# Performance work log

Hardware: AMD Instinct MI355X
Metric: run time of the kernel (lower is better)

## Reference

```python
import jax, jax.numpy as jnp
import numpy as np

NUM_CLASSES = 19
VIEWS = 50          # views_per_class: min(min_views, max_views_per_class)=50, no max_features_total cap (38*50<=10000)
TEMP = 0.1
CM_TEMP = 0.1
EPS = 1e-12


def setup_inputs() -> dict:
    key = jax.random.key(0)
    k1, k2, k3 = jax.random.split(key, 3)
    label = jax.random.randint(k1, (2, 512, 1024), 0, NUM_CLASSES)
    color_fea = jax.random.normal(k2, (2, 256, 128, 256), dtype=jnp.float32)
    other_fea = jax.random.normal(k3, (2, 256, 128, 256), dtype=jnp.float32)
    return {"label": label, "color_fea": color_fea, "other_fea": other_fea}


def _sample(compare, feature):
    # compare: [N, Cc, HW] bool (pixel belongs to class), feature: [N, C, HW]
    # random per-class sampling of VIEWS pixels: argsort random keys restricted to class pixels
    n, cc, hw = compare.shape
    rand = jax.random.uniform(jax.random.key(42), (n, hw))
    keys = jnp.where(compare, rand[:, None, :], 2.0)          # non-class pixels pushed to the end
    idx = jnp.argsort(keys, axis=-1)[:, :, :VIEWS]            # [N, Cc, V]
    samp = jnp.take_along_axis(feature[:, None, :, :], idx[:, :, None, :], axis=-1)  # [N, Cc, C, V]
    c = feature.shape[1]
    return samp.reshape(n * cc, c, VIEWS)                     # [T, C, V]


def _norm_flat(feats):
    # feats: [T, C, V] -> l2-normalize over C, transpose, flatten to [T*V, C]
    f = feats / jnp.maximum(jnp.linalg.norm(feats, axis=1, keepdims=True), EPS)
    t, c, v = f.shape
    return jnp.transpose(f, (0, 2, 1)).reshape(t * v, c)


def _masks(labels_flat):
    m = (labels_flat[:, None] == labels_flat[None, :]).astype(jnp.float32)
    neg = 1.0 - m
    pos = m * (1.0 - jnp.eye(m.shape[0], dtype=m.dtype))      # exclude self from positives
    return pos, neg


def _infonce(dot, pos, neg):
    exp = jnp.exp(dot)
    neg_logits = (exp * neg).sum(1, keepdims=True)
    log_prob = dot - jnp.log(exp + neg_logits)
    pos_sums = pos.sum(1)
    norm = jnp.where(pos_sums > 0, pos_sums, 1.0)
    return -(((pos * log_prob).sum(1)) / norm).mean()


def reference(label, color_fea, other_fea):
    n, h, w = label.shape
    scale = w // color_fea.shape[-1]
    # nearest-neighbour downsample of label to feature resolution (torch interpolate 'nearest' with integer factor)
    ld = label[:, ::scale, ::scale].reshape(n, -1)                       # [N, HW]
    compare = ld[:, None, :] == jnp.arange(NUM_CLASSES)[None, :, None]   # [N, Cc, HW]
    cf = color_fea.reshape(n, color_fea.shape[1], -1)
    of = other_fea.reshape(n, other_fea.shape[1], -1)
    fc = _sample(compare, cf)                                            # [T, C, V]
    fo = _sample(compare, of)
    labels = jnp.tile(jnp.arange(NUM_CLASSES), n).astype(jnp.float32)    # [T]
    labels_flat = jnp.repeat(labels, VIEWS)                              # [T*V]
    pos, neg = _masks(labels_flat)
    fcf = _norm_flat(fc)
    fof = _norm_flat(fo)
    loss_cm = _infonce(fcf @ fof.T / CM_TEMP, pos, neg)
    loss_vis = _infonce(fcf @ fcf.T / TEMP, pos, neg)
    loss_aux = _infonce(fof @ fof.T / TEMP, pos, neg)
    return (loss_cm, loss_vis, loss_aux)
```

## Files before the change

### kernel.cpp

```cpp
#include <hip/hip_runtime.h>
#include <hip/hip_bf16.h>
#include <cstdint>
#include <cstddef>

#define HW    32768
#define NCLS  19
#define VIEWS 50
#define NT    38
#define NR    1900
#define NRP   1920
#define CH    256
#define CAP   3072

#define OFF_LD   65536u
#define OFF_SEL  131072u
#define OFF_CNT  133120u
#define OFF_KEYS 133184u
#define OFF_FCF  366656u
#define OFF_FOF  612416u
#define OFF_NEG  858176u
#define OFF_POS  863936u

typedef __attribute__((ext_vector_type(8))) short short8;
typedef __attribute__((ext_vector_type(4))) float f32x4;

__device__ __forceinline__ unsigned rotl32(unsigned x, int d) {
    return (x << d) | (x >> (32 - d));
}

__global__ __launch_bounds__(256) void prep_kernel(const int* __restrict__ label,
                                                   int* __restrict__ ld,
                                                   int* __restrict__ counts,
                                                   unsigned long long* __restrict__ keys,
                                                   float* __restrict__ negsum,
                                                   float* __restrict__ out) {
    int tid = threadIdx.x;
    int j = blockIdx.x * 256 + tid;
    unsigned x0 = (unsigned)j, x1 = (unsigned)(j + HW);
    const unsigned ks0 = 0u, ks1 = 42u, ks2 = 0x1BD11BDAu ^ 0u ^ 42u;
    x0 += ks0; x1 += ks1;
#define TF_RND(r) { x0 += x1; x1 = rotl32(x1, r); x1 ^= x0; }
    TF_RND(13) TF_RND(15) TF_RND(26) TF_RND(6)   x0 += ks1; x1 += ks2 + 1u;
    TF_RND(17) TF_RND(29) TF_RND(16) TF_RND(24)  x0 += ks2; x1 += ks0 + 2u;
    TF_RND(13) TF_RND(15) TF_RND(26) TF_RND(6)   x0 += ks0; x1 += ks1 + 3u;
    TF_RND(17) TF_RND(29) TF_RND(16) TF_RND(24)  x0 += ks1; x1 += ks2 + 4u;
    TF_RND(13) TF_RND(15) TF_RND(26) TF_RND(6)   x0 += ks2; x1 += ks0 + 5u;
#undef TF_RND
    float r0 = __uint_as_float((x0 >> 9) | 0x3f800000u) - 1.0f;
    float r1 = __uint_as_float((x1 >> 9) | 0x3f800000u) - 1.0f;
    int y = j >> 8, x = j & 255;
    int off = (y << 2) * 1024 + (x << 2);
    int c0 = label[off];
    int c1 = label[512 * 1024 + off];
    ld[j]      = c0;
    ld[HW + j] = c1;
    if (j < 3 * NR) negsum[j] = 0.0f;
    if (j < 3) out[j] = 0.0f;

    __shared__ int lcnt[NT], lbase[NT];
    if (tid < NT) lcnt[tid] = 0;
    __syncthreads();
    int t0 = c0, t1 = NCLS + c1;
    int p0 = atomicAdd(&lcnt[t0], 1);
    int p1 = atomicAdd(&lcnt[t1], 1);
    __syncthreads();
    if (tid < NT) {
        int c = lcnt[tid];
        lbase[tid] = (c > 0) ? atomicAdd(&counts[tid], c) : 0;
    }
    __syncthreads();
    int s0 = lbase[t0] + p0;
    int s1 = lbase[t1] + p1;
    if (s0 < CAP)
        keys[(size_t)t0 * CAP + s0] = (((unsigned long long)__float_as_uint(r0)) << 32) | (unsigned)j;
    if (s1 < CAP)
        keys[(size_t)t1 * CAP + s1] = (((unsigned long long)__float_as_uint(r1)) << 32) | (unsigned)j;
}

__global__ __launch_bounds__(256) void select_kernel(const int* __restrict__ counts,
                                                     const unsigned long long* __restrict__ keys,
                                                     const int* __restrict__ ld,
                                                     int* __restrict__ sel) {
    int t = blockIdx.x;
    int tid = threadIdx.x;
    int cnt = min(counts[t], CAP);
    const unsigned long long* g = keys + (size_t)t * CAP;
    __shared__ unsigned hist[256];
    __shared__ unsigned long long cand[256];
    __shared__ int s_B, s_nbelow, s_ncand;
    hist[tid] = 0;
    if (tid == 0) { s_B = 256; s_nbelow = 0; s_ncand = 0; }
    __syncthreads();

    unsigned long long kreg[12];
    int binreg[12];
    int nk = 0;
    for (int p = tid; p < cnt; p += 256) {
        unsigned long long k = g[p];
        unsigned v = (unsigned)(__uint_as_float((unsigned)(k >> 32)) * 8388608.0f);
        int b = (int)(v >> 15);
        kreg[nk] = k; binreg[nk] = b; nk++;
        atomicAdd(&hist[b], 1u);
    }
    __syncthreads();

    if (cnt >= VIEWS) {
        for (int s = 1; s < 256; s <<= 1) {
            unsigned add = (tid >= s) ? hist[tid - s] : 0u;
            unsigned cur = hist[tid];
            __syncthreads();
            hist[tid] = cur + add;
            __syncthreads();
        }
        unsigned cum  = hist[tid];
        unsigned prev = (tid > 0) ? hist[tid - 1] : 0u;
        if (cum >= VIEWS && prev < VIEWS) s_B = tid;
        __syncthreads();
        int B = s_B;
        for (int q = 0; q < nk; ++q) {
            if (binreg[q] < B) {
                int pos = atomicAdd(&s_nbelow, 1);
                if (pos < VIEWS) sel[t * VIEWS + pos] = (int)(kreg[q] & 0xffffffffu);
            } else if (binreg[q] == B) {
                int pos = atomicAdd(&s_ncand, 1);
                if (pos < 256) cand[pos] = kreg[q];
            }
        }
        __syncthreads();
        int nbelow = s_nbelow;
        int need   = VIEWS - nbelow;
        int ncand  = min(s_ncand, 256);
        if (tid < 64) {
            unsigned long long r0 = (tid       < ncand) ? cand[tid]       : ~0ull;
            unsigned long long r1 = (tid + 64  < ncand) ? cand[tid + 64]  : ~0ull;
            unsigned long long r2 = (tid + 128 < ncand) ? cand[tid + 128] : ~0ull;
            unsigned long long r3 = (tid + 192 < ncand) ? cand[tid + 192] : ~0ull;
            for (int v = 0; v < need; ++v) {
                unsigned long long a = (r0 < r1) ? r0 : r1;
                unsigned long long b = (r2 < r3) ? r2 : r3;
                unsigned long long best = (a < b) ? a : b;
                for (int m = 32; m >= 1; m >>= 1) {
                    unsigned long long o = __shfl_xor(best, m);
                    if (o < best) best = o;
                }
                if (tid == 0) sel[t * VIEWS + nbelow + v] = (int)(best & 0xffffffffu);
                if (r0 == best) r0 = ~0ull;
                if (r1 == best) r1 = ~0ull;
                if (r2 == best) r2 = ~0ull;
                if (r3 == best) r3 = ~0ull;
            }
        }
    } else {
        for (int q = 0; q < nk; ++q) {
            int pos = atomicAdd(&s_nbelow, 1);
            if (pos < VIEWS) sel[t * VIEWS + pos] = (int)(kreg[q] & 0xffffffffu);
        }
        __syncthreads();
        if (tid == 0) {
            int fill = s_nbelow;
            int n = t / NCLS, c = t % NCLS;
            const int* ldn = ld + n * HW;
            for (int j = 0; j < HW && fill < VIEWS; ++j)
                if (ldn[j] != c) sel[t * VIEWS + fill++] = j;
        }
    }
}

__global__ __launch_bounds__(256) void gather_kernel(const float* __restrict__ cf,
                                                     const float* __restrict__ of,
                                                     const int* __restrict__ sel,
                                                     unsigned short* __restrict__ fcf,
                                                     unsigned short* __restrict__ fof) {
    int r = blockIdx.x;
    int ch = threadIdx.x;
    if (r >= NR) {
        fcf[r * CH + ch] = 0;
        fof[r * CH + ch] = 0;
        return;
    }
    int t = r / VIEWS;
    int n = t / NCLS;
    int idx = sel[r];
    float vc = cf[(size_t)(n * CH + ch) * HW + idx];
    float vo = of[(size_t)(n * CH + ch) * HW + idx];
    __shared__ float partc[4], parto[4];
    float sc = vc * vc, so = vo * vo;
    for (int m = 32; m >= 1; m >>= 1) {
        sc += __shfl_xor(sc, m);
        so += __shfl_xor(so, m);
    }
    int wave = ch >> 6, lane = ch & 63;
    if (lane == 0) { partc[wave] = sc; parto[wave] = so; }
    __syncthreads();
    float nc = fmaxf(sqrtf(partc[0] + partc[1] + partc[2] + partc[3]), 1e-12f);
    float no = fmaxf(sqrtf(parto[0] + parto[1] + parto[2] + parto[3]), 1e-12f);
    __hip_bfloat16 hc = __float2bfloat16(vc / nc);
    __hip_bfloat16 ho = __float2bfloat16(vo / no);
    fcf[r * CH + ch] = *(unsigned short*)&hc;
    fof[r * CH + ch] = *(unsigned short*)&ho;
}

#define BLDS 272
__global__ __launch_bounds__(256) void gram_kernel(const unsigned short* __restrict__ fcf,
                                                   const unsigned short* __restrict__ fof,
                                                   float* __restrict__ negsum,
                                                   float* __restrict__ posdot) {
    int z = blockIdx.z;
    bool sym = (z >= 1);
    if (sym && blockIdx.y > blockIdx.x) return;
    bool mirror = sym && (blockIdx.y < blockIdx.x);
    const unsigned short* A = (z == 2) ? fof : fcf;
    const unsigned short* B = (z == 1) ? fcf : fof;
    int i0 = blockIdx.y * 64, j0 = blockIdx.x * 64;
    int tid = threadIdx.x;
    int wave = tid >> 6, lane = tid & 63;
    __shared__ unsigned short Bs[64][BLDS];
    __shared__ float negs[64], negsB[64];
    if (tid < 64) { negs[tid] = 0.0f; negsB[tid] = 0.0f; }

    short8 breg[8];
#pragma unroll
    for (int m = 0; m < 8; ++m) {
        int e = m * 256 + tid;
        int row = e >> 5, ch = (e & 31) * 8;
        breg[m] = *(const short8*)(B + (size_t)(j0 + row) * CH + ch);
    }
    const unsigned short* pa = A + (size_t)(i0 + wave * 16 + (lane & 15)) * CH + (lane >> 4) * 8;
    short8 af[8];
#pragma unroll
    for (int k = 0; k < 8; ++k) af[k] = *(const short8*)(pa + k * 32);
#pragma unroll
    for (int m = 0; m < 8; ++m) {
        int e = m * 256 + tid;
        int row = e >> 5, ch = (e & 31) * 8;
        *(short8*)&Bs[row][ch] = breg[m];
    }
    __syncthreads();

    f32x4 acc[4] = {{0,0,0,0},{0,0,0,0},{0,0,0,0},{0,0,0,0}};
#pragma unroll
    for (int k = 0; k < 8; ++k) {
#pragma unroll
        for (int b = 0; b < 4; ++b) {
            short8 bf = *(const short8*)&Bs[b * 16 + (lane & 15)][k * 32 + (lane >> 4) * 8];
            acc[b] = __builtin_amdgcn_mfma_f32_16x16x32_bf16(af[k], bf, acc[b], 0, 0, 0);
        }
    }

    float* pd = posdot + (size_t)z * NR * 100;
    int col = lane & 15, quad = lane >> 4;
    float negB[4] = {0.0f, 0.0f, 0.0f, 0.0f};
    for (int r = 0; r < 4; ++r) {
        int irow = wave * 16 + quad * 4 + r;
        int i = i0 + irow;
        bool iok = (i < NR);
        int ci = (i / VIEWS) % NCLS;
        float negacc = 0.0f;
        for (int b = 0; b < 4; ++b) {
            int j = j0 + b * 16 + col;
            if (!iok || j >= NR) continue;
            int cj = (j / VIEWS) % NCLS;
            float d = acc[b][r] * 10.0f;
            if (ci == cj) {
                int p = (j / (NCLS * VIEWS)) * VIEWS + (j % VIEWS);
                pd[(size_t)i * 100 + p] = d;
                if (mirror) {
                    int q = (i / (NCLS * VIEWS)) * VIEWS + (i % VIEWS);
                    pd[(size_t)j * 100 + q] = d;
                }
            } else {
                float e = __expf(d);
                negacc += e;
                if (mirror) negB[b] += e;
            }
        }
        for (int m = 8; m >= 1; m >>= 1) negacc += __shfl_xor(negacc, m);
        if (col == 0 && iok) negs[irow] = negacc;
    }
    if (mirror) {
        for (int b = 0; b < 4; ++b) {
            float v = negB[b];
            v += __shfl_xor(v, 16);
            v += __shfl_xor(v, 32);
            if (quad == 0) atomicAdd(&negsB[b * 16 + col], v);
        }
    }
    __syncthreads();
    if (tid < 64) {
        int i = i0 + tid;
        if (i < NR) atomicAdd(&negsum[z * NR + i], negs[tid]);
        if (mirror) {
            int j = j0 + tid;
            if (j < NR) atomicAdd(&negsum[z * NR + j], negsB[tid]);
        }
    }
}

__global__ void finalize_kernel(const float* __restrict__ negsum,
                                const float* __restrict__ posdot,
                                float* __restrict__ out) {
    int g = blockIdx.x * 256 + threadIdx.x;
    __shared__ float part[3];
    if (threadIdx.x < 3) part[threadIdx.x] = 0.0f;
    __syncthreads();
    if (g < 3 * NR) {
        int l = g / NR, i = g % NR;
        float NL = negsum[l * NR + i];
        int pself = (i / (NCLS * VIEWS)) * VIEWS + (i % VIEWS);
        const float* pd = posdot + ((size_t)l * NR + i) * 100;
        float s = 0.0f;
        for (int p = 0; p < 100; ++p) {
            if (p == pself) continue;
            float d = pd[p];
            s += d - logf(__expf(d) + NL);
        }
        atomicAdd(&part[l], s);
    }
    __syncthreads();
    if (threadIdx.x < 3)
        atomicAdd(&out[threadIdx.x], -part[threadIdx.x] * (1.0f / (99.0f * 1900.0f)));
}

extern "C" void kernel_launch(void* const* d_in, const int* in_sizes, int n_in,
                              void* d_out, int out_size, void* d_ws, size_t ws_size,
                              hipStream_t stream) {
    (void)in_sizes; (void)n_in; (void)out_size; (void)ws_size;
    const int*   label = (const int*)d_in[0];
    const float* cf    = (const float*)d_in[1];
    const float* of    = (const float*)d_in[2];
    float* ws = (float*)d_ws;
    int*                ld     = (int*)(ws + OFF_LD);
    int*                sel    = (int*)(ws + OFF_SEL);
    int*                counts = (int*)(ws + OFF_CNT);
    unsigned long long* keys   = (unsigned long long*)(ws + OFF_KEYS);
    unsigned short*     fcf    = (unsigned short*)(ws + OFF_FCF);
    unsigned short*     fof    = (unsigned short*)(ws + OFF_FOF);
    float*              negsum = ws + OFF_NEG;
    float*              posdot = ws + OFF_POS;
    float*              out    = (float*)d_out;

    hipMemsetAsync(counts, 0, NT * sizeof(int), stream);

    prep_kernel<<<HW / 256, 256, 0, stream>>>(label, ld, counts, keys, negsum, out);
    select_kernel<<<NT, 256, 0, stream>>>(counts, keys, ld, sel);
    gather_kernel<<<NRP, 256, 0, stream>>>(cf, of, sel, fcf, fof);
    dim3 g4(NRP / 64, NRP / 64, 3);
    gram_kernel<<<g4, 256, 0, stream>>>(fcf, fof, negsum, posdot);
    finalize_kernel<<<(3 * NR + 255) / 256, 256, 0, stream>>>(negsum, posdot, out);
}
```

Baseline: 205.7 us.

## Fuse all stages into one cooperative persistent kernel with grid syncs

```diff
diff --git a/kernel.cpp b/kernel.cpp
--- a/kernel.cpp
+++ b/kernel.cpp
@@ -1,7 +1,10 @@
 #include <hip/hip_runtime.h>
 #include <hip/hip_bf16.h>
+#include <hip/hip_cooperative_groups.h>
 #include <cstdint>
 #include <cstddef>
+
+namespace cg = cooperative_groups;
 
 #define HW    32768
 #define NCLS  19
@@ -10,16 +13,20 @@
 #define NR    1900
 #define NRP   1920
 #define CH    256
-#define CAP   3072
-
-#define OFF_LD   65536u
-#define OFF_SEL  131072u
-#define OFF_CNT  133120u
-#define OFF_KEYS 133184u
-#define OFF_FCF  366656u
-#define OFF_FOF  612416u
-#define OFF_NEG  858176u
-#define OFF_POS  863936u
+#define CAPB  256
+#define CAPD  3072
+#define GDIM  512
+#define NTILE 1830
+#define BLDS  272
+
+#define OFF_LD    0u
+#define OFF_SEL   65536u
+#define OFF_CNTPB 67584u
+#define OFF_KEYS  72704u
+#define OFF_FCF   2563072u
+#define OFF_FOF   2808832u
+#define OFF_NEG   3054592u
+#define OFF_POS   3060352u
 
 typedef __attribute__((ext_vector_type(8))) short short8;
 typedef __attribute__((ext_vector_type(4))) float f32x4;
@@ -28,297 +35,318 @@
     return (x << d) | (x >> (32 - d));
 }
 
-__global__ __launch_bounds__(256) void prep_kernel(const int* __restrict__ label,
-                                                   int* __restrict__ ld,
-                                                   int* __restrict__ counts,
-                                                   unsigned long long* __restrict__ keys,
-                                                   float* __restrict__ negsum,
-                                                   float* __restrict__ out) {
+__global__ __launch_bounds__(256, 2) void fused_kernel(
+    const int* __restrict__ label, const float* __restrict__ cf, const float* __restrict__ of,
+    int* __restrict__ ld, int* __restrict__ sel, int* __restrict__ cntpb,
+    unsigned long long* __restrict__ keys, unsigned short* __restrict__ fcf,
+    unsigned short* __restrict__ fof, float* __restrict__ negsum,
+    float* __restrict__ posdot, float* __restrict__ out)
+{
+    cg::grid_group grid = cg::this_grid();
     int tid = threadIdx.x;
-    int j = blockIdx.x * 256 + tid;
-    unsigned x0 = (unsigned)j, x1 = (unsigned)(j + HW);
-    const unsigned ks0 = 0u, ks1 = 42u, ks2 = 0x1BD11BDAu ^ 0u ^ 42u;
-    x0 += ks0; x1 += ks1;
+    int b = blockIdx.x;
+
+    __shared__ __align__(16) char smem[34816];
+    __shared__ int lcnt[NT];
+    __shared__ unsigned hist[256];
+    __shared__ int s_B, s_nbelow, s_ncand;
+    __shared__ float pc4[4], po4[4];
+    __shared__ float negs[64], negsB[64];
+    __shared__ float part3[3];
+
+    if (b < 128) {
+        int j = b * 256 + tid;
+        unsigned x0 = (unsigned)j, x1 = (unsigned)(j + HW);
+        const unsigned ks0 = 0u, ks1 = 42u, ks2 = 0x1BD11BDAu ^ 0u ^ 42u;
+        x0 += ks0; x1 += ks1;
 #define TF_RND(r) { x0 += x1; x1 = rotl32(x1, r); x1 ^= x0; }
-    TF_RND(13) TF_RND(15) TF_RND(26) TF_RND(6)   x0 += ks1; x1 += ks2 + 1u;
-    TF_RND(17) TF_RND(29) TF_RND(16) TF_RND(24)  x0 += ks2; x1 += ks0 + 2u;
-    TF_RND(13) TF_RND(15) TF_RND(26) TF_RND(6)   x0 += ks0; x1 += ks1 + 3u;
-    TF_RND(17) TF_RND(29) TF_RND(16) TF_RND(24)  x0 += ks1; x1 += ks2 + 4u;
-    TF_RND(13) TF_RND(15) TF_RND(26) TF_RND(6)   x0 += ks2; x1 += ks0 + 5u;
+        TF_RND(13) TF_RND(15) TF_RND(26) TF_RND(6)   x0 += ks1; x1 += ks2 + 1u;
+        TF_RND(17) TF_RND(29) TF_RND(16) TF_RND(24)  x0 += ks2; x1 += ks0 + 2u;
+        TF_RND(13) TF_RND(15) TF_RND(26) TF_RND(6)   x0 += ks0; x1 += ks1 + 3u;
+        TF_RND(17) TF_RND(29) TF_RND(16) TF_RND(24)  x0 += ks1; x1 += ks2 + 4u;
+        TF_RND(13) TF_RND(15) TF_RND(26) TF_RND(6)   x0 += ks2; x1 += ks0 + 5u;
 #undef TF_RND
-    float r0 = __uint_as_float((x0 >> 9) | 0x3f800000u) - 1.0f;
-    float r1 = __uint_as_float((x1 >> 9) | 0x3f800000u) - 1.0f;
-    int y = j >> 8, x = j & 255;
-    int off = (y << 2) * 1024 + (x << 2);
-    int c0 = label[off];
-    int c1 = label[512 * 1024 + off];
-    ld[j]      = c0;
-    ld[HW + j] = c1;
-    if (j < 3 * NR) negsum[j] = 0.0f;
-    if (j < 3) out[j] = 0.0f;
-
-    __shared__ int lcnt[NT], lbase[NT];
-    if (tid < NT) lcnt[tid] = 0;
-    __syncthreads();
-    int t0 = c0, t1 = NCLS + c1;
-    int p0 = atomicAdd(&lcnt[t0], 1);
-    int p1 = atomicAdd(&lcnt[t1], 1);
-    __syncthreads();
-    if (tid < NT) {
-        int c = lcnt[tid];
-        lbase[tid] = (c > 0) ? atomicAdd(&counts[tid], c) : 0;
-    }
-    __syncthreads();
-    int s0 = lbase[t0] + p0;
-    int s1 = lbase[t1] + p1;
-    if (s0 < CAP)
-        keys[(size_t)t0 * CAP + s0] = (((unsigned long long)__float_as_uint(r0)) << 32) | (unsigned)j;
-    if (s1 < CAP)
-        keys[(size_t)t1 * CAP + s1] = (((unsigned long long)__float_as_uint(r1)) << 32) | (unsigned)j;
-}
-
-__global__ __launch_bounds__(256) void select_kernel(const int* __restrict__ counts,
-                                                     const unsigned long long* __restrict__ keys,
-                                                     const int* __restrict__ ld,
-                                                     int* __restrict__ sel) {
-    int t = blockIdx.x;
-    int tid = threadIdx.x;
-    int cnt = min(counts[t], CAP);
-    const unsigned long long* g = keys + (size_t)t * CAP;
-    __shared__ unsigned hist[256];
-    __shared__ unsigned long long cand[256];
-    __shared__ int s_B, s_nbelow, s_ncand;
-    hist[tid] = 0;
-    if (tid == 0) { s_B = 256; s_nbelow = 0; s_ncand = 0; }
-    __syncthreads();
-
-    unsigned long long kreg[12];
-    int binreg[12];
-    int nk = 0;
-    for (int p = tid; p < cnt; p += 256) {
-        unsigned long long k = g[p];
-        unsigned v = (unsigned)(__uint_as_float((unsigned)(k >> 32)) * 8388608.0f);
-        int b = (int)(v >> 15);
-        kreg[nk] = k; binreg[nk] = b; nk++;
-        atomicAdd(&hist[b], 1u);
-    }
-    __syncthreads();
-
-    if (cnt >= VIEWS) {
-        for (int s = 1; s < 256; s <<= 1) {
-            unsigned add = (tid >= s) ? hist[tid - s] : 0u;
-            unsigned cur = hist[tid];
-            __syncthreads();
-            hist[tid] = cur + add;
-            __syncthreads();
-        }
-        unsigned cum  = hist[tid];
-        unsigned prev = (tid > 0) ? hist[tid - 1] : 0u;
-        if (cum >= VIEWS && prev < VIEWS) s_B = tid;
-        __syncthreads();
-        int B = s_B;
-        for (int q = 0; q < nk; ++q) {
-            if (binreg[q] < B) {
+        float r0 = __uint_as_float((x0 >> 9) | 0x3f800000u) - 1.0f;
+        float r1 = __uint_as_float((x1 >> 9) | 0x3f800000u) - 1.0f;
+        int y = j >> 8, x = j & 255;
+        int off = (y << 2) * 1024 + (x << 2);
+        int c0 = label[off];
+        int c1 = label[512 * 1024 + off];
+        ld[j]      = c0;
+        ld[HW + j] = c1;
+        if (j < 3 * NR) negsum[j] = 0.0f;
+        if (j < 3) out[j] = 0.0f;
+
+        if (tid < NT) lcnt[tid] = 0;
+        __syncthreads();
+        int t0 = c0, t1 = NCLS + c1;
+        int p0 = atomicAdd(&lcnt[t0], 1);
+        int p1 = atomicAdd(&lcnt[t1], 1);
+        keys[((size_t)t0 * 128 + b) * CAPB + p0] =
+            (((unsigned long long)__float_as_uint(r0)) << 32) | (unsigned)j;
+        keys[((size_t)t1 * 128 + b) * CAPB + p1] =
+            (((unsigned long long)__float_as_uint(r1)) << 32) | (unsigned)j;
+        __syncthreads();
+        if (tid < NT) cntpb[tid * 128 + b] = lcnt[tid];
+    }
+    grid.sync();
+
+    if (b < NT) {
+        int t = b;
+        unsigned long long* dense = (unsigned long long*)smem;
+        unsigned long long* cand  = (unsigned long long*)(smem + 24576);
+        int* csc = (int*)(smem + 26624);
+
+        int mycnt = 0;
+        if (tid < 128) { mycnt = cntpb[t * 128 + tid]; csc[tid] = mycnt; }
+        hist[tid] = 0;
+        if (tid == 0) { s_B = 256; s_nbelow = 0; s_ncand = 0; }
+        __syncthreads();
+        for (int s = 1; s < 128; s <<= 1) {
+            int add = (tid < 128 && tid >= s) ? csc[tid - s] : 0;
+            __syncthreads();
+            if (tid < 128) csc[tid] += add;
+            __syncthreads();
+        }
+        int total = csc[127];
+        if (tid < 128) {
+            int excl = csc[tid] - mycnt;
+            const unsigned long long* src = keys + ((size_t)t * 128 + tid) * CAPB;
+            for (int q = 0; q < mycnt; ++q) {
+                int dst = excl + q;
+                if (dst < CAPD) dense[dst] = src[q];
+            }
+        }
+        __syncthreads();
+        int cnt = min(total, CAPD);
+
+        unsigned long long kreg[12];
+        int binreg[12];
+        int nk = 0;
+        for (int p = tid; p < cnt; p += 256) {
+            unsigned long long k = dense[p];
+            unsigned v = (unsigned)(__uint_as_float((unsigned)(k >> 32)) * 8388608.0f);
+            int bn = (int)(v >> 15);
+            kreg[nk] = k; binreg[nk] = bn; nk++;
+            atomicAdd(&hist[bn], 1u);
+        }
+        __syncthreads();
+
+        if (cnt >= VIEWS) {
+            for (int s = 1; s < 256; s <<= 1) {
+                unsigned add = (tid >= s) ? hist[tid - s] : 0u;
+                unsigned cur = hist[tid];
+                __syncthreads();
+                hist[tid] = cur + add;
+                __syncthreads();
+            }
+            unsigned cum  = hist[tid];
+            unsigned prev = (tid > 0) ? hist[tid - 1] : 0u;
+            if (cum >= VIEWS && prev < VIEWS) s_B = tid;
+            __syncthreads();
+            int B = s_B;
+            for (int q = 0; q < nk; ++q) {
+                if (binreg[q] < B) {
+                    int pos = atomicAdd(&s_nbelow, 1);
+                    if (pos < VIEWS) sel[t * VIEWS + pos] = (int)(kreg[q] & 0xffffffffu);
+                } else if (binreg[q] == B) {
+                    int pos = atomicAdd(&s_ncand, 1);
+                    if (pos < 256) cand[pos] = kreg[q];
+                }
+            }
+            __syncthreads();
+            int nbelow = s_nbelow;
+            int need   = VIEWS - nbelow;
+            int ncand  = min(s_ncand, 256);
+            if (tid < 64) {
+                unsigned long long r0 = (tid       < ncand) ? cand[tid]       : ~0ull;
+                unsigned long long r1 = (tid + 64  < ncand) ? cand[tid + 64]  : ~0ull;
+                unsigned long long r2 = (tid + 128 < ncand) ? cand[tid + 128] : ~0ull;
+                unsigned long long r3 = (tid + 192 < ncand) ? cand[tid + 192] : ~0ull;
+                for (int v = 0; v < need; ++v) {
+                    unsigned long long a = (r0 < r1) ? r0 : r1;
+                    unsigned long long bb = (r2 < r3) ? r2 : r3;
+                    unsigned long long best = (a < bb) ? a : bb;
+                    for (int m = 32; m >= 1; m >>= 1) {
+                        unsigned long long o = __shfl_xor(best, m);
+                        if (o < best) best = o;
+                    }
+                    if (tid == 0) sel[t * VIEWS + nbelow + v] = (int)(best & 0xffffffffu);
+                    if (r0 == best) r0 = ~0ull;
+                    if (r1 == best) r1 = ~0ull;
+                    if (r2 == best) r2 = ~0ull;
+                    if (r3 == best) r3 = ~0ull;
+                }
+            }
+        } else {
+            for (int q = 0; q < nk; ++q) {
                 int pos = atomicAdd(&s_nbelow, 1);
                 if (pos < VIEWS) sel[t * VIEWS + pos] = (int)(kreg[q] & 0xffffffffu);
-            } else if (binreg[q] == B) {
-                int pos = atomicAdd(&s_ncand, 1);
-                if (pos < 256) cand[pos] = kreg[q];
-            }
-        }
-        __syncthreads();
-        int nbelow = s_nbelow;
-        int need   = VIEWS - nbelow;
-        int ncand  = min(s_ncand, 256);
+            }
+            __syncthreads();
+            if (tid == 0) {
+                int fill = s_nbelow;
+                int n = t / NCLS, c = t % NCLS;
+                const int* ldn = ld + n * HW;
+                for (int j = 0; j < HW && fill < VIEWS; ++j)
+                    if (ldn[j] != c) sel[t * VIEWS + fill++] = j;
+            }
+        }
+    }
+    grid.sync();
+
+    for (int r = b; r < NRP; r += GDIM) {
+        int ch = tid;
+        if (r >= NR) {
+            fcf[r * CH + ch] = 0;
+            fof[r * CH + ch] = 0;
+        } else {
+            int t = r / VIEWS;
+            int n = t / NCLS;
+            int idx = sel[r];
+            float vc = cf[(size_t)(n * CH + ch) * HW + idx];
+            float vo = of[(size_t)(n * CH + ch) * HW + idx];
+            float sc = vc * vc, so = vo * vo;
+            for (int m = 32; m >= 1; m >>= 1) {
+                sc += __shfl_xor(sc, m);
+                so += __shfl_xor(so, m);
+            }
+            int wave = ch >> 6, lane = ch & 63;
+            if (lane == 0) { pc4[wave] = sc; po4[wave] = so; }
+            __syncthreads();
+            float nc = fmaxf(sqrtf(pc4[0] + pc4[1] + pc4[2] + pc4[3]), 1e-12f);
+            float no = fmaxf(sqrtf(po4[0] + po4[1] + po4[2] + po4[3]), 1e-12f);
+            __hip_bfloat16 hc = __float2bfloat16(vc / nc);
+            __hip_bfloat16 ho = __float2bfloat16(vo / no);
+            fcf[r * CH + ch] = *(unsigned short*)&hc;
+            fof[r * CH + ch] = *(unsigned short*)&ho;
+            __syncthreads();
+        }
+    }
+    grid.sync();
+
+    for (int T = b; T < NTILE; T += GDIM) {
+        int z, by, bx;
+        if (T < 900) { z = 0; by = T / 30; bx = T % 30; }
+        else {
+            int u = T - 900;
+            z = 1 + u / 465;
+            int v = u % 465;
+            int rr_ = 0, acc_ = 0;
+            while (acc_ + (30 - rr_) <= v) { acc_ += 30 - rr_; ++rr_; }
+            by = rr_; bx = rr_ + (v - acc_);
+        }
+        bool mirror = (z >= 1) && (by < bx);
+        const unsigned short* A  = (z == 2) ? fof : fcf;
+        const unsigned short* Bp = (z == 1) ? fcf : fof;
+        int i0 = by * 64, j0 = bx * 64;
+        int wave = tid >> 6, lane = tid & 63;
+        unsigned short (*Bs)[BLDS] = (unsigned short (*)[BLDS])(void*)smem;
+        if (tid < 64) { negs[tid] = 0.0f; negsB[tid] = 0.0f; }
+
+        short8 breg[8];
+#pragma unroll
+        for (int m = 0; m < 8; ++m) {
+            int e = m * 256 + tid;
+            int row = e >> 5, chc = (e & 31) * 8;
+            breg[m] = *(const short8*)(Bp + (size_t)(j0 + row) * CH + chc);
+        }
+        const unsigned short* pa = A + (size_t)(i0 + wave * 16 + (lane & 15)) * CH + (lane >> 4) * 8;
+        short8 af[8];
+#pragma unroll
+        for (int k = 0; k < 8; ++k) af[k] = *(const short8*)(pa + k * 32);
+#pragma unroll
+        for (int m = 0; m < 8; ++m) {
+            int e = m * 256 + tid;
+            int row = e >> 5, chc = (e & 31) * 8;
+            *(short8*)&Bs[row][chc] = breg[m];
+        }
+        __syncthreads();
+
+        f32x4 acc[4] = {{0,0,0,0},{0,0,0,0},{0,0,0,0},{0,0,0,0}};
+#pragma unroll
+        for (int k = 0; k < 8; ++k) {
+#pragma unroll
+            for (int bb = 0; bb < 4; ++bb) {
+                short8 bf = *(const short8*)&Bs[bb * 16 + (lane & 15)][k * 32 + (lane >> 4) * 8];
+                acc[bb] = __builtin_amdgcn_mfma_f32_16x16x32_bf16(af[k], bf, acc[bb], 0, 0, 0);
+            }
+        }
+
+        float* pd = posdot + (size_t)z * NR * 100;
+        int col = lane & 15, quad = lane >> 4;
+        float negB4[4] = {0.0f, 0.0f, 0.0f, 0.0f};
+#pragma unroll
+        for (int rr = 0; rr < 4; ++rr) {
+            int irow = wave * 16 + quad * 4 + rr;
+            int i = i0 + irow;
+            bool iok = (i < NR);
+            int ci = (i / VIEWS) % NCLS;
+            float negacc = 0.0f;
+#pragma unroll
+            for (int bb = 0; bb < 4; ++bb) {
+                int jj = j0 + bb * 16 + col;
+                if (!iok || jj >= NR) continue;
+                int cj = (jj / VIEWS) % NCLS;
+                float d = acc[bb][rr] * 10.0f;
+                if (ci == cj) {
+                    int p = (jj / (NCLS * VIEWS)) * VIEWS + (jj % VIEWS);
+                    pd[(size_t)i * 100 + p] = d;
+                    if (mirror) {
+                        int q = (i / (NCLS * VIEWS)) * VIEWS + (i % VIEWS);
+                        pd[(size_t)jj * 100 + q] = d;
+                    }
+                } else {
+                    float e = __expf(d);
+                    negacc += e;
+                    if (mirror) negB4[bb] += e;
+                }
+            }
+            for (int m = 8; m >= 1; m >>= 1) negacc += __shfl_xor(negacc, m);
+            if (col == 0 && iok) negs[irow] = negacc;
+        }
+        if (mirror) {
+#pragma unroll
+            for (int bb = 0; bb < 4; ++bb) {
+                float v = negB4[bb];
+                v += __shfl_xor(v, 16);
+                v += __shfl_xor(v, 32);
+                if (quad == 0) atomicAdd(&negsB[bb * 16 + col], v);
+            }
+        }
+        __syncthreads();
         if (tid < 64) {
-            unsigned long long r0 = (tid       < ncand) ? cand[tid]       : ~0ull;
-            unsigned long long r1 = (tid + 64  < ncand) ? cand[tid + 64]  : ~0ull;
-            unsigned long long r2 = (tid + 128 < ncand) ? cand[tid + 128] : ~0ull;
-            unsigned long long r3 = (tid + 192 < ncand) ? cand[tid + 192] : ~0ull;
-            for (int v = 0; v < need; ++v) {
-                unsigned long long a = (r0 < r1) ? r0 : r1;
-                unsigned long long b = (r2 < r3) ? r2 : r3;
-                unsigned long long best = (a < b) ? a : b;
-                for (int m = 32; m >= 1; m >>= 1) {
-                    unsigned long long o = __shfl_xor(best, m);
-                    if (o < best) best = o;
-                }
-                if (tid == 0) sel[t * VIEWS + nbelow + v] = (int)(best & 0xffffffffu);
-                if (r0 == best) r0 = ~0ull;
-                if (r1 == best) r1 = ~0ull;
-                if (r2 == best) r2 = ~0ull;
-                if (r3 == best) r3 = ~0ull;
-            }
-        }
-    } else {
-        for (int q = 0; q < nk; ++q) {
-            int pos = atomicAdd(&s_nbelow, 1);
-            if (pos < VIEWS) sel[t * VIEWS + pos] = (int)(kreg[q] & 0xffffffffu);
-        }
-        __syncthreads();
-        if (tid == 0) {
-            int fill = s_nbelow;
-            int n = t / NCLS, c = t % NCLS;
-            const int* ldn = ld + n * HW;
-            for (int j = 0; j < HW && fill < VIEWS; ++j)
-                if (ldn[j] != c) sel[t * VIEWS + fill++] = j;
-        }
-    }
-}
-
-__global__ __launch_bounds__(256) void gather_kernel(const float* __restrict__ cf,
-                                                     const float* __restrict__ of,
-                                                     const int* __restrict__ sel,
-                                                     unsigned short* __restrict__ fcf,
-                                                     unsigned short* __restrict__ fof) {
-    int r = blockIdx.x;
-    int ch = threadIdx.x;
-    if (r >= NR) {
-        fcf[r * CH + ch] = 0;
-        fof[r * CH + ch] = 0;
-        return;
-    }
-    int t = r / VIEWS;
-    int n = t / NCLS;
-    int idx = sel[r];
-    float vc = cf[(size_t)(n * CH + ch) * HW + idx];
-    float vo = of[(size_t)(n * CH + ch) * HW + idx];
-    __shared__ float partc[4], parto[4];
-    float sc = vc * vc, so = vo * vo;
-    for (int m = 32; m >= 1; m >>= 1) {
-        sc += __shfl_xor(sc, m);
-        so += __shfl_xor(so, m);
-    }
-    int wave = ch >> 6, lane = ch & 63;
-    if (lane == 0) { partc[wave] = sc; parto[wave] = so; }
-    __syncthreads();
-    float nc = fmaxf(sqrtf(partc[0] + partc[1] + partc[2] + partc[3]), 1e-12f);
-    float no = fmaxf(sqrtf(parto[0] + parto[1] + parto[2] + parto[3]), 1e-12f);
-    __hip_bfloat16 hc = __float2bfloat16(vc / nc);
-    __hip_bfloat16 ho = __float2bfloat16(vo / no);
-    fcf[r * CH + ch] = *(unsigned short*)&hc;
-    fof[r * CH + ch] = *(unsigned short*)&ho;
-}
-
-#define BLDS 272
-__global__ __launch_bounds__(256) void gram_kernel(const unsigned short* __restrict__ fcf,
-                                                   const unsigned short* __restrict__ fof,
-                                                   float* __restrict__ negsum,
-                                                   float* __restrict__ posdot) {
-    int z = blockIdx.z;
-    bool sym = (z >= 1);
-    if (sym && blockIdx.y > blockIdx.x) return;
-    bool mirror = sym && (blockIdx.y < blockIdx.x);
-    const unsigned short* A = (z == 2) ? fof : fcf;
-    const unsigned short* B = (z == 1) ? fcf : fof;
-    int i0 = blockIdx.y * 64, j0 = blockIdx.x * 64;
-    int tid = threadIdx.x;
-    int wave = tid >> 6, lane = tid & 63;
-    __shared__ unsigned short Bs[64][BLDS];
-    __shared__ float negs[64], negsB[64];
-    if (tid < 64) { negs[tid] = 0.0f; negsB[tid] = 0.0f; }
-
-    short8 breg[8];
-#pragma unroll
-    for (int m = 0; m < 8; ++m) {
-        int e = m * 256 + tid;
-        int row = e >> 5, ch = (e & 31) * 8;
-        breg[m] = *(const short8*)(B + (size_t)(j0 + row) * CH + ch);
-    }
-    const unsigned short* pa = A + (size_t)(i0 + wave * 16 + (lane & 15)) * CH + (lane >> 4) * 8;
-    short8 af[8];
-#pragma unroll
-    for (int k = 0; k < 8; ++k) af[k] = *(const short8*)(pa + k * 32);
-#pragma unroll
-    for (int m = 0; m < 8; ++m) {
-        int e = m * 256 + tid;
-        int row = e >> 5, ch = (e & 31) * 8;
-        *(short8*)&Bs[row][ch] = breg[m];
-    }
-    __syncthreads();
-
-    f32x4 acc[4] = {{0,0,0,0},{0,0,0,0},{0,0,0,0},{0,0,0,0}};
-#pragma unroll
-    for (int k = 0; k < 8; ++k) {
-#pragma unroll
-        for (int b = 0; b < 4; ++b) {
-            short8 bf = *(const short8*)&Bs[b * 16 + (lane & 15)][k * 32 + (lane >> 4) * 8];
-            acc[b] = __builtin_amdgcn_mfma_f32_16x16x32_bf16(af[k], bf, acc[b], 0, 0, 0);
-        }
-    }
-
-    float* pd = posdot + (size_t)z * NR * 100;
-    int col = lane & 15, quad = lane >> 4;
-    float negB[4] = {0.0f, 0.0f, 0.0f, 0.0f};
-    for (int r = 0; r < 4; ++r) {
-        int irow = wave * 16 + quad * 4 + r;
-        int i = i0 + irow;
-        bool iok = (i < NR);
-        int ci = (i / VIEWS) % NCLS;
-        float negacc = 0.0f;
-        for (int b = 0; b < 4; ++b) {
-            int j = j0 + b * 16 + col;
-            if (!iok || j >= NR) continue;
-            int cj = (j / VIEWS) % NCLS;
-            float d = acc[b][r] * 10.0f;
-            if (ci == cj) {
-                int p = (j / (NCLS * VIEWS)) * VIEWS + (j % VIEWS);
-                pd[(size_t)i * 100 + p] = d;
-                if (mirror) {
-                    int q = (i / (NCLS * VIEWS)) * VIEWS + (i % VIEWS);
-                    pd[(size_t)j * 100 + q] = d;
-                }
-            } else {
-                float e = __expf(d);
-                negacc += e;
-                if (mirror) negB[b] += e;
-            }
-        }
-        for (int m = 8; m >= 1; m >>= 1) negacc += __shfl_xor(negacc, m);
-        if (col == 0 && iok) negs[irow] = negacc;
-    }
-    if (mirror) {
-        for (int b = 0; b < 4; ++b) {
-            float v = negB[b];
-            v += __shfl_xor(v, 16);
-            v += __shfl_xor(v, 32);
-            if (quad == 0) atomicAdd(&negsB[b * 16 + col], v);
-        }
-    }
-    __syncthreads();
-    if (tid < 64) {
-        int i = i0 + tid;
-        if (i < NR) atomicAdd(&negsum[z * NR + i], negs[tid]);
-        if (mirror) {
-            int j = j0 + tid;
-            if (j < NR) atomicAdd(&negsum[z * NR + j], negsB[tid]);
-        }
-    }
-}
-
-__global__ void finalize_kernel(const float* __restrict__ negsum,
-                                const float* __restrict__ posdot,
-                                float* __restrict__ out) {
-    int g = blockIdx.x * 256 + threadIdx.x;
-    __shared__ float part[3];
-    if (threadIdx.x < 3) part[threadIdx.x] = 0.0f;
-    __syncthreads();
-    if (g < 3 * NR) {
-        int l = g / NR, i = g % NR;
-        float NL = negsum[l * NR + i];
-        int pself = (i / (NCLS * VIEWS)) * VIEWS + (i % VIEWS);
-        const float* pd = posdot + ((size_t)l * NR + i) * 100;
-        float s = 0.0f;
-        for (int p = 0; p < 100; ++p) {
-            if (p == pself) continue;
-            float d = pd[p];
-            s += d - logf(__expf(d) + NL);
-        }
-        atomicAdd(&part[l], s);
-    }
-    __syncthreads();
-    if (threadIdx.x < 3)
-        atomicAdd(&out[threadIdx.x], -part[threadIdx.x] * (1.0f / (99.0f * 1900.0f)));
+            int i = i0 + tid;
+            if (i < NR) atomicAdd(&negsum[z * NR + i], negs[tid]);
+            if (mirror) {
+                int jj = j0 + tid;
+                if (jj < NR) atomicAdd(&negsum[z * NR + jj], negsB[tid]);
+            }
+        }
+    }
+    grid.sync();
+
+    if (b < 23) {
+        int g = b * 256 + tid;
+        if (tid < 3) part3[tid] = 0.0f;
+        __syncthreads();
+        if (g < 3 * NR) {
+            int l = g / NR, i = g % NR;
+            float NL = negsum[l * NR + i];
+            int pself = (i / (NCLS * VIEWS)) * VIEWS + (i % VIEWS);
+            const float* pdp = posdot + ((size_t)l * NR + i) * 100;
+            float s = 0.0f;
+            for (int p = 0; p < 100; ++p) {
+                if (p == pself) continue;
+                float d = pdp[p];
+                s += d - logf(__expf(d) + NL);
+            }
+            atomicAdd(&part3[l], s);
+        }
+        __syncthreads();
+        if (tid < 3)
+            atomicAdd(&out[tid], -part3[tid] * (1.0f / (99.0f * 1900.0f)));
+    }
 }
 
 extern "C" void kernel_launch(void* const* d_in, const int* in_sizes, int n_in,
@@ -331,7 +359,7 @@
     float* ws = (float*)d_ws;
     int*                ld     = (int*)(ws + OFF_LD);
     int*                sel    = (int*)(ws + OFF_SEL);
-    int*                counts = (int*)(ws + OFF_CNT);
+    int*                cntpb  = (int*)(ws + OFF_CNTPB);
     unsigned long long* keys   = (unsigned long long*)(ws + OFF_KEYS);
     unsigned short*     fcf    = (unsigned short*)(ws + OFF_FCF);
     unsigned short*     fof    = (unsigned short*)(ws + OFF_FOF);
@@ -339,12 +367,9 @@
     float*              posdot = ws + OFF_POS;
     float*              out    = (float*)d_out;
 
-    hipMemsetAsync(counts, 0, NT * sizeof(int), stream);
-
-    prep_kernel<<<HW / 256, 256, 0, stream>>>(label, ld, counts, keys, negsum, out);
-    select_kernel<<<NT, 256, 0, stream>>>(counts, keys, ld, sel);
-    gather_kernel<<<NRP, 256, 0, stream>>>(cf, of, sel, fcf, fof);
-    dim3 g4(NRP / 64, NRP / 64, 3);
-    gram_kernel<<<g4, 256, 0, stream>>>(fcf, fof, negsum, posdot);
-    finalize_kernel<<<(3 * NR + 255) / 256, 256, 0, stream>>>(negsum, posdot, out);
+    void* args[] = {(void*)&label, (void*)&cf, (void*)&of, (void*)&ld, (void*)&sel,
+                    (void*)&cntpb, (void*)&keys, (void*)&fcf, (void*)&fof,
+                    (void*)&negsum, (void*)&posdot, (void*)&out};
+    hipLaunchCooperativeKernel((const void*)fused_kernel, dim3(GDIM), dim3(256),
+                               args, 0, stream);
 }
```

Measured after the change: 449.4 us. 2.18x slower.

## Fuse label prep and per-class selection into one sampling kernel with LDS buffers

Applied to the files above, without the earlier changes.

```diff
diff --git a/kernel.cpp b/kernel.cpp
--- a/kernel.cpp
+++ b/kernel.cpp
@@ -10,16 +10,13 @@
 #define NR    1900
 #define NRP   1920
 #define CH    256
-#define CAP   3072
-
-#define OFF_LD   65536u
-#define OFF_SEL  131072u
-#define OFF_CNT  133120u
-#define OFF_KEYS 133184u
-#define OFF_FCF  366656u
-#define OFF_FOF  612416u
-#define OFF_NEG  858176u
-#define OFF_POS  863936u
+#define CAPS  2560
+
+#define OFF_SEL 0u
+#define OFF_NEG 2048u
+#define OFF_POS 7808u
+#define OFF_FCF 577856u
+#define OFF_FOF 823616u
 
 typedef __attribute__((ext_vector_type(8))) short short8;
 typedef __attribute__((ext_vector_type(4))) float f32x4;
@@ -28,79 +25,54 @@
     return (x << d) | (x >> (32 - d));
 }
 
-__global__ __launch_bounds__(256) void prep_kernel(const int* __restrict__ label,
-                                                   int* __restrict__ ld,
-                                                   int* __restrict__ counts,
-                                                   unsigned long long* __restrict__ keys,
-                                                   float* __restrict__ negsum,
-                                                   float* __restrict__ out) {
-    int tid = threadIdx.x;
-    int j = blockIdx.x * 256 + tid;
-    unsigned x0 = (unsigned)j, x1 = (unsigned)(j + HW);
-    const unsigned ks0 = 0u, ks1 = 42u, ks2 = 0x1BD11BDAu ^ 0u ^ 42u;
-    x0 += ks0; x1 += ks1;
+__global__ __launch_bounds__(256) void sample_kernel(const int* __restrict__ label,
+                                                     int* __restrict__ sel,
+                                                     float* __restrict__ negsum,
+                                                     float* __restrict__ out) {
+    int t = blockIdx.x, tid = threadIdx.x;
+    int n = t / NCLS, c = t % NCLS;
+    __shared__ unsigned long long dense[CAPS];
+    __shared__ unsigned long long cand[256];
+    __shared__ unsigned hist[256];
+    __shared__ int s_cnt, s_B, s_nbelow, s_ncand;
+    hist[tid] = 0;
+    if (tid == 0) { s_cnt = 0; s_B = 256; s_nbelow = 0; s_ncand = 0; }
+    if (tid < 150) negsum[t * 150 + tid] = 0.0f;
+    if (t == 0 && tid < 3) out[tid] = 0.0f;
+    __syncthreads();
+
+    const int* lab = label + (size_t)n * 512 * 1024;
+    for (int j = tid; j < HW; j += 256) {
+        int lv = lab[((j >> 8) << 2) * 1024 + ((j & 255) << 2)];
+        if (lv != c) continue;
+        unsigned x0 = (unsigned)j, x1 = (unsigned)(j + HW);
+        const unsigned ks0 = 0u, ks1 = 42u, ks2 = 0x1BD11BDAu ^ 0u ^ 42u;
+        x0 += ks0; x1 += ks1;
 #define TF_RND(r) { x0 += x1; x1 = rotl32(x1, r); x1 ^= x0; }
-    TF_RND(13) TF_RND(15) TF_RND(26) TF_RND(6)   x0 += ks1; x1 += ks2 + 1u;
-    TF_RND(17) TF_RND(29) TF_RND(16) TF_RND(24)  x0 += ks2; x1 += ks0 + 2u;
-    TF_RND(13) TF_RND(15) TF_RND(26) TF_RND(6)   x0 += ks0; x1 += ks1 + 3u;
-    TF_RND(17) TF_RND(29) TF_RND(16) TF_RND(24)  x0 += ks1; x1 += ks2 + 4u;
-    TF_RND(13) TF_RND(15) TF_RND(26) TF_RND(6)   x0 += ks2; x1 += ks0 + 5u;
+        TF_RND(13) TF_RND(15) TF_RND(26) TF_RND(6)   x0 += ks1; x1 += ks2 + 1u;
+        TF_RND(17) TF_RND(29) TF_RND(16) TF_RND(24)  x0 += ks2; x1 += ks0 + 2u;
+        TF_RND(13) TF_RND(15) TF_RND(26) TF_RND(6)   x0 += ks0; x1 += ks1 + 3u;
+        TF_RND(17) TF_RND(29) TF_RND(16) TF_RND(24)  x0 += ks1; x1 += ks2 + 4u;
+        TF_RND(13) TF_RND(15) TF_RND(26) TF_RND(6)   x0 += ks2; x1 += ks0 + 5u;
 #undef TF_RND
-    float r0 = __uint_as_float((x0 >> 9) | 0x3f800000u) - 1.0f;
-    float r1 = __uint_as_float((x1 >> 9) | 0x3f800000u) - 1.0f;
-    int y = j >> 8, x = j & 255;
-    int off = (y << 2) * 1024 + (x << 2);
-    int c0 = label[off];
-    int c1 = label[512 * 1024 + off];
-    ld[j]      = c0;
-    ld[HW + j] = c1;
-    if (j < 3 * NR) negsum[j] = 0.0f;
-    if (j < 3) out[j] = 0.0f;
-
-    __shared__ int lcnt[NT], lbase[NT];
-    if (tid < NT) lcnt[tid] = 0;
-    __syncthreads();
-    int t0 = c0, t1 = NCLS + c1;
-    int p0 = atomicAdd(&lcnt[t0], 1);
-    int p1 = atomicAdd(&lcnt[t1], 1);
-    __syncthreads();
-    if (tid < NT) {
-        int c = lcnt[tid];
-        lbase[tid] = (c > 0) ? atomicAdd(&counts[tid], c) : 0;
-    }
-    __syncthreads();
-    int s0 = lbase[t0] + p0;
-    int s1 = lbase[t1] + p1;
-    if (s0 < CAP)
-        keys[(size_t)t0 * CAP + s0] = (((unsigned long long)__float_as_uint(r0)) << 32) | (unsigned)j;
-    if (s1 < CAP)
-        keys[(size_t)t1 * CAP + s1] = (((unsigned long long)__float_as_uint(r1)) << 32) | (unsigned)j;
-}
-
-__global__ __launch_bounds__(256) void select_kernel(const int* __restrict__ counts,
-                                                     const unsigned long long* __restrict__ keys,
-                                                     const int* __restrict__ ld,
-                                                     int* __restrict__ sel) {
-    int t = blockIdx.x;
-    int tid = threadIdx.x;
-    int cnt = min(counts[t], CAP);
-    const unsigned long long* g = keys + (size_t)t * CAP;
-    __shared__ unsigned hist[256];
-    __shared__ unsigned long long cand[256];
-    __shared__ int s_B, s_nbelow, s_ncand;
-    hist[tid] = 0;
-    if (tid == 0) { s_B = 256; s_nbelow = 0; s_ncand = 0; }
-    __syncthreads();
+        unsigned xb = n ? x1 : x0;
+        float r = __uint_as_float((xb >> 9) | 0x3f800000u) - 1.0f;
+        int pos = atomicAdd(&s_cnt, 1);
+        if (pos < CAPS)
+            dense[pos] = (((unsigned long long)__float_as_uint(r)) << 32) | (unsigned)j;
+    }
+    __syncthreads();
+    int cnt = min(s_cnt, CAPS);
 
     unsigned long long kreg[12];
     int binreg[12];
     int nk = 0;
     for (int p = tid; p < cnt; p += 256) {
-        unsigned long long k = g[p];
+        unsigned long long k = dense[p];
         unsigned v = (unsigned)(__uint_as_float((unsigned)(k >> 32)) * 8388608.0f);
-        int b = (int)(v >> 15);
-        kreg[nk] = k; binreg[nk] = b; nk++;
-        atomicAdd(&hist[b], 1u);
+        int bn = (int)(v >> 15);
+        kreg[nk] = k; binreg[nk] = bn; nk++;
+        atomicAdd(&hist[bn], 1u);
     }
     __syncthreads();
 
@@ -158,10 +130,10 @@
         __syncthreads();
         if (tid == 0) {
             int fill = s_nbelow;
-            int n = t / NCLS, c = t % NCLS;
-            const int* ldn = ld + n * HW;
-            for (int j = 0; j < HW && fill < VIEWS; ++j)
-                if (ldn[j] != c) sel[t * VIEWS + fill++] = j;
+            for (int j = 0; j < HW && fill < VIEWS; ++j) {
+                int lv = lab[((j >> 8) << 2) * 1024 + ((j & 255) << 2)];
+                if (lv != c) sel[t * VIEWS + fill++] = j;
+            }
         }
     }
 }
@@ -329,22 +301,16 @@
     const float* cf    = (const float*)d_in[1];
     const float* of    = (const float*)d_in[2];
     float* ws = (float*)d_ws;
-    int*                ld     = (int*)(ws + OFF_LD);
-    int*                sel    = (int*)(ws + OFF_SEL);
-    int*                counts = (int*)(ws + OFF_CNT);
-    unsigned long long* keys   = (unsigned long long*)(ws + OFF_KEYS);
-    unsigned short*     fcf    = (unsigned short*)(ws + OFF_FCF);
-    unsigned short*     fof    = (unsigned short*)(ws + OFF_FOF);
-    float*              negsum = ws + OFF_NEG;
-    float*              posdot = ws + OFF_POS;
-    float*              out    = (float*)d_out;
-
-    hipMemsetAsync(counts, 0, NT * sizeof(int), stream);
-
-    prep_kernel<<<HW / 256, 256, 0, stream>>>(label, ld, counts, keys, negsum, out);
-    select_kernel<<<NT, 256, 0, stream>>>(counts, keys, ld, sel);
+    int*            sel    = (int*)(ws + OFF_SEL);
+    float*          negsum = ws + OFF_NEG;
+    float*          posdot = ws + OFF_POS;
+    unsigned short* fcf    = (unsigned short*)(ws + OFF_FCF);
+    unsigned short* fof    = (unsigned short*)(ws + OFF_FOF);
+    float*          out    = (float*)d_out;
+
+    sample_kernel<<<NT, 256, 0, stream>>>(label, sel, negsum, out);
     gather_kernel<<<NRP, 256, 0, stream>>>(cf, of, sel, fcf, fof);
-    dim3 g4(NRP / 64, NRP / 64, 3);
-    gram_kernel<<<g4, 256, 0, stream>>>(fcf, fof, negsum, posdot);
+    dim3 g3(NRP / 64, NRP / 64, 3);
+    gram_kernel<<<g3, 256, 0, stream>>>(fcf, fof, negsum, posdot);
     finalize_kernel<<<(3 * NR + 255) / 256, 256, 0, stream>>>(negsum, posdot, out);
 }
```

New measurement: 277.8 us. 1.35x slower.

## Replace global atomic bucketing with per-block key buckets and compact triangular grid

Applied to the files above, without the earlier changes.

```diff
diff --git a/kernel.cpp b/kernel.cpp
--- a/kernel.cpp
+++ b/kernel.cpp
@@ -10,16 +10,17 @@
 #define NR    1900
 #define NRP   1920
 #define CH    256
-#define CAP   3072
-
-#define OFF_LD   65536u
-#define OFF_SEL  131072u
-#define OFF_CNT  133120u
-#define OFF_KEYS 133184u
-#define OFF_FCF  366656u
-#define OFF_FOF  612416u
-#define OFF_NEG  858176u
-#define OFF_POS  863936u
+#define CAPB  256
+#define CAPD  3072
+#define NTILE 1830
+
+#define OFF_SEL   0u
+#define OFF_CNTPB 2048u
+#define OFF_KEYS  7168u
+#define OFF_FCF   2497536u
+#define OFF_FOF   2743296u
+#define OFF_NEG   2989056u
+#define OFF_POS   2994816u
 
 typedef __attribute__((ext_vector_type(8))) short short8;
 typedef __attribute__((ext_vector_type(4))) float f32x4;
@@ -29,13 +30,17 @@
 }
 
 __global__ __launch_bounds__(256) void prep_kernel(const int* __restrict__ label,
-                                                   int* __restrict__ ld,
-                                                   int* __restrict__ counts,
+                                                   int* __restrict__ cntpb,
                                                    unsigned long long* __restrict__ keys,
                                                    float* __restrict__ negsum,
                                                    float* __restrict__ out) {
-    int tid = threadIdx.x;
-    int j = blockIdx.x * 256 + tid;
+    int b = blockIdx.x, tid = threadIdx.x;
+    __shared__ int lcnt[NT];
+
+    { int q = b * 45 + tid; if (tid < 45 && q < 3 * NR) negsum[q] = 0.0f; }
+    if (b == 0 && tid < 3) out[tid] = 0.0f;
+
+    int j = b * 256 + tid;
     unsigned x0 = (unsigned)j, x1 = (unsigned)(j + HW);
     const unsigned ks0 = 0u, ks1 = 42u, ks2 = 0x1BD11BDAu ^ 0u ^ 42u;
     x0 += ks0; x1 += ks1;
@@ -52,55 +57,63 @@
     int off = (y << 2) * 1024 + (x << 2);
     int c0 = label[off];
     int c1 = label[512 * 1024 + off];
-    ld[j]      = c0;
-    ld[HW + j] = c1;
-    if (j < 3 * NR) negsum[j] = 0.0f;
-    if (j < 3) out[j] = 0.0f;
-
-    __shared__ int lcnt[NT], lbase[NT];
+
     if (tid < NT) lcnt[tid] = 0;
     __syncthreads();
     int t0 = c0, t1 = NCLS + c1;
     int p0 = atomicAdd(&lcnt[t0], 1);
     int p1 = atomicAdd(&lcnt[t1], 1);
-    __syncthreads();
-    if (tid < NT) {
-        int c = lcnt[tid];
-        lbase[tid] = (c > 0) ? atomicAdd(&counts[tid], c) : 0;
-    }
-    __syncthreads();
-    int s0 = lbase[t0] + p0;
-    int s1 = lbase[t1] + p1;
-    if (s0 < CAP)
-        keys[(size_t)t0 * CAP + s0] = (((unsigned long long)__float_as_uint(r0)) << 32) | (unsigned)j;
-    if (s1 < CAP)
-        keys[(size_t)t1 * CAP + s1] = (((unsigned long long)__float_as_uint(r1)) << 32) | (unsigned)j;
-}
-
-__global__ __launch_bounds__(256) void select_kernel(const int* __restrict__ counts,
+    keys[((size_t)t0 * 128 + b) * CAPB + p0] =
+        (((unsigned long long)__float_as_uint(r0)) << 32) | (unsigned)j;
+    keys[((size_t)t1 * 128 + b) * CAPB + p1] =
+        (((unsigned long long)__float_as_uint(r1)) << 32) | (unsigned)j;
+    __syncthreads();
+    if (tid < NT) cntpb[tid * 128 + b] = lcnt[tid];
+}
+
+__global__ __launch_bounds__(256) void select_kernel(const int* __restrict__ cntpb,
                                                      const unsigned long long* __restrict__ keys,
-                                                     const int* __restrict__ ld,
+                                                     const int* __restrict__ label,
                                                      int* __restrict__ sel) {
-    int t = blockIdx.x;
-    int tid = threadIdx.x;
-    int cnt = min(counts[t], CAP);
-    const unsigned long long* g = keys + (size_t)t * CAP;
+    int t = blockIdx.x, tid = threadIdx.x;
+    __shared__ unsigned long long dense[CAPD];
+    __shared__ unsigned long long cand[256];
     __shared__ unsigned hist[256];
-    __shared__ unsigned long long cand[256];
+    __shared__ int csc[128];
     __shared__ int s_B, s_nbelow, s_ncand;
+
+    int mycnt = 0;
+    if (tid < 128) { mycnt = cntpb[t * 128 + tid]; csc[tid] = mycnt; }
     hist[tid] = 0;
     if (tid == 0) { s_B = 256; s_nbelow = 0; s_ncand = 0; }
     __syncthreads();
+    for (int s = 1; s < 128; s <<= 1) {
+        int add = (tid < 128 && tid >= s) ? csc[tid - s] : 0;
+        __syncthreads();
+        if (tid < 128) csc[tid] += add;
+        __syncthreads();
+    }
+    int total = csc[127];
+    if (tid < 128) {
+        int excl = csc[tid] - mycnt;
+        const unsigned long long* src = keys + ((size_t)t * 128 + tid) * CAPB;
+        for (int q = 0; q < mycnt; ++q) {
+            int dst = excl + q;
+            if (dst < CAPD) dense[dst] = src[q];
+        }
+    }
+    __syncthreads();
+    int cnt = min(total, CAPD);
 
     unsigned long long kreg[12];
     int binreg[12];
     int nk = 0;
     for (int p = tid; p < cnt; p += 256) {
-        unsigned long long k = g[p];
+        unsigned long long k = dense[p];
         unsigned v = (unsigned)(__uint_as_float((unsigned)(k >> 32)) * 8388608.0f);
-        int b = (int)(v >> 15);
-        kreg[nk] = k; binreg[nk] = b; nk++;
-        atomicAdd(&hist[b], 1u);
+        int bn = (int)(v >> 15);
+        kreg[nk] = k; binreg[nk] = bn; nk++;
+        atomicAdd(&hist[bn], 1u);
     }
     __syncthreads();
 
@@ -137,8 +150,8 @@
             unsigned long long r3 = (tid + 192 < ncand) ? cand[tid + 192] : ~0ull;
             for (int v = 0; v < need; ++v) {
                 unsigned long long a = (r0 < r1) ? r0 : r1;
-                unsigned long long b = (r2 < r3) ? r2 : r3;
-                unsigned long long best = (a < b) ? a : b;
+                unsigned long long bb = (r2 < r3) ? r2 : r3;
+                unsigned long long best = (a < bb) ? a : bb;
                 for (int m = 32; m >= 1; m >>= 1) {
                     unsigned long long o = __shfl_xor(best, m);
                     if (o < best) best = o;
@@ -159,9 +172,11 @@
         if (tid == 0) {
             int fill = s_nbelow;
             int n = t / NCLS, c = t % NCLS;
-            const int* ldn = ld + n * HW;
-            for (int j = 0; j < HW && fill < VIEWS; ++j)
-                if (ldn[j] != c) sel[t * VIEWS + fill++] = j;
+            const int* lab = label + (size_t)n * 512 * 1024;
+            for (int jj = 0; jj < HW && fill < VIEWS; ++jj) {
+                int lv = lab[((jj >> 8) << 2) * 1024 + ((jj & 255) << 2)];
+                if (lv != c) sel[t * VIEWS + fill++] = jj;
+            }
         }
     }
 }
@@ -205,13 +220,21 @@
                                                    const unsigned short* __restrict__ fof,
                                                    float* __restrict__ negsum,
                                                    float* __restrict__ posdot) {
-    int z = blockIdx.z;
-    bool sym = (z >= 1);
-    if (sym && blockIdx.y > blockIdx.x) return;
-    bool mirror = sym && (blockIdx.y < blockIdx.x);
+    int T = blockIdx.x;
+    int z, by, bx;
+    if (T < 900) { z = 0; by = T / 30; bx = T % 30; }
+    else {
+        int u = T - 900;
+        z = 1 + u / 465;
+        int v = u % 465;
+        int rr_ = 0, acc_ = 0;
+        while (acc_ + (30 - rr_) <= v) { acc_ += 30 - rr_; ++rr_; }
+        by = rr_; bx = rr_ + (v - acc_);
+    }
+    bool mirror = (z >= 1) && (by < bx);
     const unsigned short* A = (z == 2) ? fof : fcf;
     const unsigned short* B = (z == 1) ? fcf : fof;
-    int i0 = blockIdx.y * 64, j0 = blockIdx.x * 64;
+    int i0 = by * 64, j0 = bx * 64;
     int tid = threadIdx.x;
     int wave = tid >> 6, lane = tid & 63;
     __shared__ unsigned short Bs[64][BLDS];
@@ -329,9 +352,8 @@
     const float* cf    = (const float*)d_in[1];
     const float* of    = (const float*)d_in[2];
     float* ws = (float*)d_ws;
-    int*                ld     = (int*)(ws + OFF_LD);
     int*                sel    = (int*)(ws + OFF_SEL);
-    int*                counts = (int*)(ws + OFF_CNT);
+    int*                cntpb  = (int*)(ws + OFF_CNTPB);
     unsigned long long* keys   = (unsigned long long*)(ws + OFF_KEYS);
     unsigned short*     fcf    = (unsigned short*)(ws + OFF_FCF);
     unsigned short*     fof    = (unsigned short*)(ws + OFF_FOF);
@@ -339,12 +361,9 @@
     float*              posdot = ws + OFF_POS;
     float*              out    = (float*)d_out;
 
-    hipMemsetAsync(counts, 0, NT * sizeof(int), stream);
-
-    prep_kernel<<<HW / 256, 256, 0, stream>>>(label, ld, counts, keys, negsum, out);
-    select_kernel<<<NT, 256, 0, stream>>>(counts, keys, ld, sel);
+    prep_kernel<<<128, 256, 0, stream>>>(label, cntpb, keys, negsum, out);
+    select_kernel<<<NT, 256, 0, stream>>>(cntpb, keys, label, sel);
     gather_kernel<<<NRP, 256, 0, stream>>>(cf, of, sel, fcf, fof);
-    dim3 g4(NRP / 64, NRP / 64, 3);
-    gram_kernel<<<g4, 256, 0, stream>>>(fcf, fof, negsum, posdot);
+    gram_kernel<<<NTILE, 256, 0, stream>>>(fcf, fof, negsum, posdot);
     finalize_kernel<<<(3 * NR + 255) / 256, 256, 0, stream>>>(negsum, posdot, out);
 }
```

New measurement: 203.6 us. About the same (-1.0%).
